# Kernel tuning notes

Measured on AMD Instinct MI355X. Metric: run time of the kernel, lower is better.

The kernel has to match this reference:

```python
import jax, jax.numpy as jnp
import numpy as np

D_IN = 2048
NUM_HEADS = 32
NUM_KV = 8
HEAD_DIM = 64
V_HEAD_DIM = 64
SEQ = 2048
BATCH = 1
EPS = 1e-6
NEG = -1e30


def setup_inputs() -> dict:
    key = jax.random.key(0)
    ks = jax.random.split(key, 10)
    x = jax.random.normal(ks[0], (BATCH, SEQ, D_IN), dtype=jnp.float32)
    # causal mask: True = masked out (upper triangle above diagonal)
    mask = jnp.triu(jnp.ones((SEQ, SEQ), dtype=jnp.bool_), k=1)
    # RoPE tables
    inv_freq = 1.0 / (10000.0 ** (jnp.arange(0, HEAD_DIM, 2, dtype=jnp.float32) / HEAD_DIM))
    t = jnp.arange(SEQ, dtype=jnp.float32)
    freqs = jnp.outer(t, inv_freq)  # (S, hd/2)
    emb = jnp.concatenate([freqs, freqs], axis=-1)  # (S, hd)
    cos = jnp.cos(emb)
    sin = jnp.sin(emb)
    scale = 0.02
    wq = jax.random.normal(ks[1], (D_IN, NUM_HEADS * HEAD_DIM), dtype=jnp.float32) * scale
    wk = jax.random.normal(ks[2], (D_IN, NUM_KV * HEAD_DIM), dtype=jnp.float32) * scale
    wv = jax.random.normal(ks[3], (D_IN, NUM_KV * V_HEAD_DIM), dtype=jnp.float32) * scale
    wo = jax.random.normal(ks[4], (NUM_HEADS * V_HEAD_DIM, D_IN), dtype=jnp.float32) * scale
    q_norm_w = jnp.ones((HEAD_DIM,), dtype=jnp.float32)
    k_norm_w = jnp.ones((HEAD_DIM,), dtype=jnp.float32)
    sink = jax.random.normal(ks[5], (NUM_HEADS,), dtype=jnp.float32) * 0.02
    return {"x": x, "mask": mask, "cos": cos, "sin": sin, "wq": wq, "wk": wk,
            "wv": wv, "wo": wo, "q_norm_w": q_norm_w, "k_norm_w": k_norm_w, "sink": sink}


def _rmsnorm(x, w):
    var = jnp.mean(jnp.square(x), axis=-1, keepdims=True)
    return x * jax.lax.rsqrt(var + EPS) * w


def _rope(x, cos, sin):
    # x: (b, h, s, d); cos/sin: (s, d)
    d = x.shape[-1]
    x1, x2 = x[..., : d // 2], x[..., d // 2:]
    rot = jnp.concatenate([-x2, x1], axis=-1)
    return x * cos[None, None] + rot * sin[None, None]


def reference(x, mask, cos, sin, wq, wk, wv, wo, q_norm_w, k_norm_w, sink):
    b, s, _ = x.shape
    rep = NUM_HEADS // NUM_KV
    q = (x @ wq).reshape(b, s, NUM_HEADS, HEAD_DIM).transpose(0, 2, 1, 3)
    k = (x @ wk).reshape(b, s, NUM_KV, HEAD_DIM).transpose(0, 2, 1, 3)
    v = (x @ wv).reshape(b, s, NUM_KV, V_HEAD_DIM).transpose(0, 2, 1, 3)
    q = _rope(_rmsnorm(q, q_norm_w), cos, sin)
    k = _rope(_rmsnorm(k, k_norm_w), cos, sin)
    k = jnp.repeat(k, rep, axis=1)  # (b, H, s, hd)
    v = jnp.repeat(v, rep, axis=1)  # (b, H, s, vd)
    scores = jnp.einsum('bhqd,bhkd->bhqk', q, k) * (HEAD_DIM ** -0.5)
    scores = jnp.where(mask[:s, :s], NEG, scores)
    # append learnable sink logit per head
    sink_col = jnp.broadcast_to(sink.reshape(1, NUM_HEADS, 1, 1), (b, NUM_HEADS, s, 1))
    scores = jnp.concatenate([scores, sink_col], axis=-1)
    weights = jax.nn.softmax(scores, axis=-1)[..., :-1]  # drop sink column
    out = jnp.einsum('bhqk,bhkd->bhqd', weights, v)
    out = out.transpose(0, 2, 1, 3).reshape(b, s, NUM_HEADS * V_HEAD_DIM)
    return out @ wo
```

## Files before the change

### kernel.cpp

```cpp
#include <hip/hip_runtime.h>

typedef unsigned short u16;
typedef __bf16 bf16;
typedef float f32x4 __attribute__((ext_vector_type(4)));
typedef bf16 bf16x8 __attribute__((ext_vector_type(8)));
typedef short s16x4 __attribute__((ext_vector_type(4)));
typedef u16 u16x4 __attribute__((ext_vector_type(4)));
typedef u16 u16x8 __attribute__((ext_vector_type(8)));

#define SEQ 2048
#define LOG2E 1.4426950408889634f

__device__ __forceinline__ u16 f2bf(float f) {
    return __builtin_bit_cast(u16, (bf16)f);
}
__device__ __forceinline__ float bf2f(u16 u) {
    unsigned int w = ((unsigned int)u) << 16;
    return __builtin_bit_cast(float, w);
}

__global__ __launch_bounds__(256) void cast_bf16_k(const float* __restrict__ in,
                                                   u16* __restrict__ out, int n4) {
    int i = blockIdx.x * 256 + threadIdx.x;
    int stride = gridDim.x * 256;
    for (; i < n4; i += stride) {
        float4 v = reinterpret_cast<const float4*>(in)[i];
        u16x4 o;
        o[0] = f2bf(v.x); o[1] = f2bf(v.y); o[2] = f2bf(v.z); o[3] = f2bf(v.w);
        reinterpret_cast<u16x4*>(out)[i] = o;
    }
}

__global__ __launch_bounds__(256) void transpose_cast_k(const float* __restrict__ src,
                                                        u16* __restrict__ dst, int R, int C) {
    __shared__ float t[64][65];
    int c0 = blockIdx.x * 64, r0 = blockIdx.y * 64;
    int tx = threadIdx.x & 63, ty = threadIdx.x >> 6;
#pragma unroll
    for (int i = 0; i < 16; ++i) {
        int r = ty + i * 4;
        t[r][tx] = src[(size_t)(r0 + r) * C + c0 + tx];
    }
    __syncthreads();
#pragma unroll
    for (int i = 0; i < 16; ++i) {
        int c = ty + i * 4;
        dst[(size_t)(c0 + c) * R + r0 + tx] = f2bf(t[tx][c]);
    }
}

__global__ __launch_bounds__(256) void gemm_bt_dbuf_k(const u16* __restrict__ A,
                                                      const u16* __restrict__ Bt,
                                                      u16* __restrict__ Cp,
                                                      int M, int N, int K) {
    __shared__ __align__(16) u16 As[2][128 * 32];
    __shared__ __align__(16) u16 Bs[2][128 * 32];
    int tid = threadIdx.x;
    int wave = tid >> 6, lane = tid & 63;
    int bm = blockIdx.y * 128, bn = blockIdx.x * 128;
    int z = blockIdx.z;
    int kt0 = z * (K >> 1), ktend = kt0 + (K >> 1);
    int wm = (wave >> 1) * 64, wn = (wave & 1) * 64;
    int g = lane >> 4, cidx = lane & 15;
    f32x4 acc[4][4] = {};

    int srow = lane >> 2;
    int skol = ((lane & 3) ^ ((srow >> 1) & 3)) * 8;
    int sl8 = (g ^ ((cidx >> 1) & 3)) * 8;

#define STAGE(buf, kt)                                                                \
    {                                                                                 \
        _Pragma("unroll")                                                             \
        for (int j = 0; j < 2; ++j) {                                                 \
            const u16* gpa = A + (size_t)(bm + (wave * 2 + j) * 16 + srow) * K + (kt) + skol; \
            __builtin_amdgcn_global_load_lds(                                         \
                (__attribute__((address_space(1))) void*)gpa,                         \
                (__attribute__((address_space(3))) void*)&As[buf][(wave * 2 + j) * 512], \
                16, 0, 0);                                                            \
        }                                                                             \
        _Pragma("unroll")                                                             \
        for (int j = 0; j < 2; ++j) {                                                 \
            const u16* gpb = Bt + (size_t)(bn + (wave * 2 + j) * 16 + srow) * K + (kt) + skol; \
            __builtin_amdgcn_global_load_lds(                                         \
                (__attribute__((address_space(1))) void*)gpb,                         \
                (__attribute__((address_space(3))) void*)&Bs[buf][(wave * 2 + j) * 512], \
                16, 0, 0);                                                            \
        }                                                                             \
    }

    STAGE(0, kt0);
    asm volatile("s_waitcnt vmcnt(0)" ::: "memory");
    __syncthreads();

    int cur = 0;
#pragma unroll 1
    for (int kt = kt0; kt < ktend; kt += 32) {
        if (kt + 32 < ktend) STAGE(cur ^ 1, kt + 32);

        bf16x8 af[4], bfr[4];
#pragma unroll
        for (int mi = 0; mi < 4; ++mi)
            af[mi] = *reinterpret_cast<const bf16x8*>(&As[cur][(wm + mi * 16 + cidx) * 32 + sl8]);
#pragma unroll
        for (int ni = 0; ni < 4; ++ni)
            bfr[ni] = *reinterpret_cast<const bf16x8*>(&Bs[cur][(wn + ni * 16 + cidx) * 32 + sl8]);
#pragma unroll
        for (int mi = 0; mi < 4; ++mi)
#pragma unroll
            for (int ni = 0; ni < 4; ++ni)
                acc[mi][ni] = __builtin_amdgcn_mfma_f32_16x16x32_bf16(af[mi], bfr[ni], acc[mi][ni], 0, 0, 0);

        asm volatile("s_waitcnt vmcnt(0)" ::: "memory");
        __syncthreads();
        cur ^= 1;
    }
#undef STAGE

    u16* cbase = Cp + (size_t)z * M * N;
#pragma unroll
    for (int mi = 0; mi < 4; ++mi) {
#pragma unroll
        for (int r = 0; r < 4; ++r) {
            int row = bm + wm + mi * 16 + g * 4 + r;
            u16* cp = cbase + (size_t)row * N + bn + wn + cidx;
#pragma unroll
            for (int ni = 0; ni < 4; ++ni)
                cp[ni * 16] = f2bf(acc[mi][ni][r]);
        }
    }
}

__global__ __launch_bounds__(256) void sum2_f32_k(const u16* __restrict__ a,
                                                  const u16* __restrict__ b,
                                                  float* __restrict__ out, int n8) {
    int i = blockIdx.x * 256 + threadIdx.x;
    if (i >= n8) return;
    u16x8 va = reinterpret_cast<const u16x8*>(a)[i];
    u16x8 vb = reinterpret_cast<const u16x8*>(b)[i];
    f32x4 lo, hi;
#pragma unroll
    for (int j = 0; j < 4; ++j) {
        lo[j] = bf2f(va[j]) + bf2f(vb[j]);
        hi[j] = bf2f(va[4 + j]) + bf2f(vb[4 + j]);
    }
    reinterpret_cast<f32x4*>(out)[i * 2] = lo;
    reinterpret_cast<f32x4*>(out)[i * 2 + 1] = hi;
}

__global__ __launch_bounds__(256) void norm_rope_k(const u16* __restrict__ p0,
                                                   const u16* __restrict__ p1,
                                                   const float* __restrict__ cosb,
                                                   const float* __restrict__ sinb,
                                                   const float* __restrict__ qw,
                                                   const float* __restrict__ kw,
                                                   u16* __restrict__ qn,
                                                   u16* __restrict__ kfrag) {
    int idx = blockIdx.x * 4 + (threadIdx.x >> 6);
    int lane = threadIdx.x & 63;
    int s = idx / 40, hh = idx - s * 40;
    size_t off = (hh < 32) ? ((size_t)s * 3072 + hh * 64 + lane)
                           : ((size_t)s * 3072 + 2048 + (hh - 32) * 64 + lane);
    float val = bf2f(p0[off]) + bf2f(p1[off]);
    float ss = val * val;
#pragma unroll
    for (int mm = 32; mm; mm >>= 1) ss += __shfl_xor(ss, mm);
    float w = (hh < 32) ? qw[lane] : kw[lane];
    float xn = val * rsqrtf(ss * (1.f / 64.f) + 1e-6f) * w;
    float part = __shfl_xor(xn, 32);
    float rot = (lane < 32) ? -part : part;
    float o = xn * cosb[s * 64 + lane] + rot * sinb[s * 64 + lane];
    if (hh < 32) {
        qn[(size_t)s * 2048 + hh * 64 + lane] = f2bf(o * (0.125f * LOG2E));
    } else {
        int h8 = hh - 32;
        kfrag[(((size_t)h8 * 128 + (s >> 4)) << 10) + (lane >> 3) * 128 + (s & 15) * 8 + (lane & 7)] = f2bf(o);
    }
}

__global__ __launch_bounds__(256) void v_frag_k(const u16* __restrict__ p0,
                                                const u16* __restrict__ p1,
                                                u16* __restrict__ vfrag) {
    __shared__ float t[64][65];
    int s0 = blockIdx.x * 64;
    int h = blockIdx.y;
    int tx = threadIdx.x & 63, ty = threadIdx.x >> 6;
#pragma unroll
    for (int i = 0; i < 16; ++i) {
        int r = ty + i * 4;
        size_t off = (size_t)(s0 + r) * 3072 + 2560 + h * 64 + tx;
        t[r][tx] = bf2f(p0[off]) + bf2f(p1[off]);
    }
    __syncthreads();
    int dt = threadIdx.x >> 6, g = (threadIdx.x >> 4) & 3, cc = threadIdx.x & 15;
#pragma unroll
    for (int kb2 = 0; kb2 < 4; ++kb2) {
        u16x4 o;
#pragma unroll
        for (int i = 0; i < 4; ++i) o[i] = f2bf(t[kb2 * 16 + g * 4 + i][dt * 16 + cc]);
        size_t idx = ((size_t)h * 64 + (s0 >> 5) + (kb2 >> 1)) * 2048 + dt * 512 + g * 128 + cc * 8 + (kb2 & 1) * 4;
        *reinterpret_cast<u16x4*>(&vfrag[idx]) = o;
    }
}

__global__ __launch_bounds__(256, 4) void attn_k(const u16* __restrict__ qn,
                                                 const u16* __restrict__ kfrag,
                                                 const u16* __restrict__ vfrag,
                                                 u16* __restrict__ obuf,
                                                 float* __restrict__ lbuf) {
    int h = blockIdx.x;
    int wave = threadIdx.x >> 6, lane = threadIdx.x & 63;
    int j = blockIdx.y * 4 + wave;
    int c, w;
    if (j < 32)       { c = j;                    w = 0; }
    else if (j < 96)  { c = 32 + ((j - 32) >> 1); w = (j - 32) & 1; }
    else if (j < 192) { int r = j - 96;  int q = r / 3; c = 64 + q; w = r - 3 * q; }
    else              { c = 96 + ((j - 192) >> 2); w = (j - 192) & 3; }

    int q0 = c * 16;
    int nk = q0 + 16;
    int kv0 = w * 512;
    int kvend = (kv0 + 512 < nk) ? (kv0 + 512) : nk;

    int kvh = h >> 2, g = lane >> 4, cc = lane & 15;
    int qrow = q0 + cc;

    const size_t qoff = (size_t)qrow * 2048 + h * 64;
    bf16x8 q_0 = *reinterpret_cast<const bf16x8*>(&qn[qoff + g * 8]);
    bf16x8 q_1 = *reinterpret_cast<const bf16x8*>(&qn[qoff + 32 + g * 8]);

    float l = 0.f;
    f32x4 o[4] = {};

    const u16* kbase = kfrag + (((size_t)kvh * 128) << 10) + lane * 8;
    const u16* vbase = vfrag + (size_t)kvh * 64 * 2048 + g * 128 + cc * 8;

    bf16x8 kf0[4], kf1[4];
#pragma unroll
    for (int sub = 0; sub < 4; ++sub) {
        const u16* kp = kbase + (size_t)((kv0 >> 4) + sub) * 1024;
        kf0[sub] = *reinterpret_cast<const bf16x8*>(kp);
        kf1[sub] = *reinterpret_cast<const bf16x8*>(kp + 512);
    }

#pragma unroll 1
    for (; kv0 < kvend; kv0 += 64) {
        f32x4 st[4];
        __builtin_amdgcn_s_setprio(1);
#pragma unroll
        for (int sub = 0; sub < 4; ++sub) {
            st[sub] = __builtin_amdgcn_mfma_f32_16x16x32_bf16(kf0[sub], q_0, (f32x4){0.f, 0.f, 0.f, 0.f}, 0, 0, 0);
            st[sub] = __builtin_amdgcn_mfma_f32_16x16x32_bf16(kf1[sub], q_1, st[sub], 0, 0, 0);
        }
        __builtin_amdgcn_s_setprio(0);

        if (kv0 + 64 < kvend) {
#pragma unroll
            for (int sub = 0; sub < 4; ++sub) {
                const u16* kp = kbase + (size_t)(((kv0 + 64) >> 4) + sub) * 1024;
                kf0[sub] = *reinterpret_cast<const bf16x8*>(kp);
                kf1[sub] = *reinterpret_cast<const bf16x8*>(kp + 512);
            }
        }

        bf16x8 vv[2][4];
#pragma unroll
        for (int sp = 0; sp < 2; ++sp)
#pragma unroll
            for (int dt = 0; dt < 4; ++dt)
                vv[sp][dt] = *reinterpret_cast<const bf16x8*>(
                    vbase + (size_t)((kv0 >> 5) + sp) * 2048 + dt * 512);

        if (kv0 + 64 > q0) {
#pragma unroll
            for (int sub = 0; sub < 4; ++sub)
#pragma unroll
                for (int r = 0; r < 4; ++r)
                    if (kv0 + sub * 16 + g * 4 + r > qrow) st[sub][r] = -1e30f;
        }

        s16x4 pf[4];
        float rs = 0.f;
#pragma unroll
        for (int sub = 0; sub < 4; ++sub)
#pragma unroll
            for (int r = 0; r < 4; ++r) {
                float e = __builtin_amdgcn_exp2f(st[sub][r]);
                rs += e;
                pf[sub][r] = (short)f2bf(e);
            }
        l += rs;

        __builtin_amdgcn_s_setprio(1);
#pragma unroll
        for (int sp = 0; sp < 2; ++sp)
#pragma unroll
            for (int dt = 0; dt < 4; ++dt) {
                s16x4 vlo = __builtin_bit_cast(s16x4,
                    __builtin_shufflevector(vv[sp][dt], vv[sp][dt], 0, 1, 2, 3));
                s16x4 vhi = __builtin_bit_cast(s16x4,
                    __builtin_shufflevector(vv[sp][dt], vv[sp][dt], 4, 5, 6, 7));
                o[dt] = __builtin_amdgcn_mfma_f32_16x16x16bf16_1k(vlo, pf[sp * 2], o[dt], 0, 0, 0);
                o[dt] = __builtin_amdgcn_mfma_f32_16x16x16bf16_1k(vhi, pf[sp * 2 + 1], o[dt], 0, 0, 0);
            }
        __builtin_amdgcn_s_setprio(0);
    }

    l += __shfl_xor(l, 16);
    l += __shfl_xor(l, 32);
    size_t slot = (size_t)h * 320 + j;
    if (lane < 16) lbuf[slot * 16 + cc] = l;
    u16* sp = obuf + slot * 1024;
#pragma unroll
    for (int dt = 0; dt < 4; ++dt) {
        u16x4 ov;
#pragma unroll
        for (int r = 0; r < 4; ++r) ov[r] = f2bf(o[dt][r]);
        *reinterpret_cast<u16x4*>(&sp[cc * 64 + dt * 16 + g * 4]) = ov;
    }
}

__global__ __launch_bounds__(256) void merge_k(const u16* __restrict__ obuf,
                                               const float* __restrict__ lbuf,
                                               const float* __restrict__ sink,
                                               u16* __restrict__ attnb) {
    int row = blockIdx.x;
    int c = row >> 4, cc = row & 15;
    int nw = (c >> 5) + 1;
    int jb = (c < 32) ? c
           : (c < 64) ? 32 + ((c - 32) << 1)
           : (c < 96) ? 96 + 3 * (c - 64)
                      : 192 + ((c - 96) << 2);
    int t = threadIdx.x;
    int h = t >> 3, col0 = (t & 7) * 8;

    float acc[8] = {};
    float lsum = __builtin_amdgcn_exp2f(sink[h] * LOG2E);
#pragma unroll 1
    for (int w = 0; w < nw; ++w) {
        size_t slot = (size_t)h * 320 + jb + w;
        lsum += lbuf[slot * 16 + cc];
        u16x8 v = *reinterpret_cast<const u16x8*>(&obuf[slot * 1024 + cc * 64 + col0]);
#pragma unroll
        for (int i = 0; i < 8; ++i) acc[i] += bf2f(v[i]);
    }
    float inv = 1.f / lsum;
    u16x8 ob;
#pragma unroll
    for (int i = 0; i < 8; ++i) ob[i] = f2bf(acc[i] * inv);
    *reinterpret_cast<u16x8*>(&attnb[(size_t)row * 2048 + h * 64 + col0]) = ob;
}

extern "C" void kernel_launch(void* const* d_in, const int* in_sizes, int n_in,
                              void* d_out, int out_size, void* d_ws, size_t ws_size,
                              hipStream_t stream) {
    const float* x    = (const float*)d_in[0];
    const float* cosb = (const float*)d_in[2];
    const float* sinb = (const float*)d_in[3];
    const float* wq   = (const float*)d_in[4];
    const float* wk   = (const float*)d_in[5];
    const float* wv   = (const float*)d_in[6];
    const float* wo   = (const float*)d_in[7];
    const float* qw   = (const float*)d_in[8];
    const float* kw   = (const float*)d_in[9];
    const float* sink = (const float*)d_in[10];
    float* out = (float*)d_out;

    char* ws = (char*)d_ws;
    size_t off = 0;
    auto alloc = [&](size_t bytes) {
        char* p = ws + off;
        off += (bytes + 255) & ~(size_t)255;
        return p;
    };
    u16*   xb    = (u16*)alloc((size_t)2048 * 2048 * 2);
    u16*   wqkvt = (u16*)alloc((size_t)3072 * 2048 * 2);
    u16*   wot   = (u16*)alloc((size_t)2048 * 2048 * 2);
    u16*   p0    = (u16*)alloc((size_t)2048 * 3072 * 2);
    u16*   p1    = (u16*)alloc((size_t)2048 * 3072 * 2);
    u16*   qnb   = (u16*)alloc((size_t)2048 * 2048 * 2);
    u16*   kfrag = (u16*)alloc((size_t)8 * 128 * 1024 * 2);
    u16*   vfrag = (u16*)alloc((size_t)8 * 64 * 2048 * 2);
    float* lbuf  = (float*)alloc((size_t)32 * 320 * 16 * 4);
    u16*   attnb = xb;
    u16*   obuf  = p0;
    u16*   o2p   = p0;

    cast_bf16_k<<<2048, 256, 0, stream>>>(x, xb, 2048 * 2048 / 4);
    transpose_cast_k<<<dim3(32, 32), 256, 0, stream>>>(wq, wqkvt, 2048, 2048);
    transpose_cast_k<<<dim3(8, 32), 256, 0, stream>>>(wk, wqkvt + (size_t)2048 * 2048, 2048, 512);
    transpose_cast_k<<<dim3(8, 32), 256, 0, stream>>>(wv, wqkvt + (size_t)2560 * 2048, 2048, 512);
    transpose_cast_k<<<dim3(32, 32), 256, 0, stream>>>(wo, wot, 2048, 2048);

    gemm_bt_dbuf_k<<<dim3(24, 16, 2), 256, 0, stream>>>(xb, wqkvt, p0, 2048, 3072, 2048);
    norm_rope_k<<<20480, 256, 0, stream>>>(p0, p1, cosb, sinb, qw, kw, qnb, kfrag);
    v_frag_k<<<dim3(32, 8), 256, 0, stream>>>(p0, p1, vfrag);

    attn_k<<<dim3(32, 80), 256, 0, stream>>>(qnb, kfrag, vfrag, obuf, lbuf);
    merge_k<<<2048, 256, 0, stream>>>(obuf, lbuf, sink, attnb);

    gemm_bt_dbuf_k<<<dim3(16, 16, 2), 256, 0, stream>>>(attnb, wot, o2p, 2048, 2048, 2048);
    sum2_f32_k<<<2048, 256, 0, stream>>>(o2p, o2p + (size_t)2048 * 2048, out, 2048 * 2048 / 8);
}
```

Measured before the change: 162.6 us.

## Use 16x16x32 MFMA for PV by permuting K/V fragment layouts; reverse block order

```diff
diff --git a/kernel.cpp b/kernel.cpp
--- a/kernel.cpp
+++ b/kernel.cpp
@@ -173,7 +173,10 @@
         qn[(size_t)s * 2048 + hh * 64 + lane] = f2bf(o * (0.125f * LOG2E));
     } else {
         int h8 = hh - 32;
-        kfrag[(((size_t)h8 * 128 + (s >> 4)) << 10) + (lane >> 3) * 128 + (s & 15) * 8 + (lane & 7)] = f2bf(o);
+        int k32 = s & 31;
+        int p32 = ((k32 >> 2) & 1) * 16 + ((k32 >> 3) << 2) + (k32 & 3);
+        int p = (s & ~31) + p32;
+        kfrag[(((size_t)h8 * 128 + (p >> 4)) << 10) + (lane >> 3) * 128 + (p & 15) * 8 + (lane & 7)] = f2bf(o);
     }
 }
 
@@ -193,12 +196,12 @@
     __syncthreads();
     int dt = threadIdx.x >> 6, g = (threadIdx.x >> 4) & 3, cc = threadIdx.x & 15;
 #pragma unroll
-    for (int kb2 = 0; kb2 < 4; ++kb2) {
-        u16x4 o;
-#pragma unroll
-        for (int i = 0; i < 4; ++i) o[i] = f2bf(t[kb2 * 16 + g * 4 + i][dt * 16 + cc]);
-        size_t idx = ((size_t)h * 64 + (s0 >> 5) + (kb2 >> 1)) * 2048 + dt * 512 + g * 128 + cc * 8 + (kb2 & 1) * 4;
-        *reinterpret_cast<u16x4*>(&vfrag[idx]) = o;
+    for (int kb = 0; kb < 2; ++kb) {
+        u16x8 o;
+#pragma unroll
+        for (int i = 0; i < 8; ++i) o[i] = f2bf(t[kb * 32 + g * 8 + i][dt * 16 + cc]);
+        *reinterpret_cast<u16x8*>(
+            &vfrag[((size_t)h * 64 + (s0 >> 5) + kb) * 2048 + dt * 512 + (size_t)(threadIdx.x & 63) * 8]) = o;
     }
 }
 
@@ -209,7 +212,7 @@
                                                  float* __restrict__ lbuf) {
     int h = blockIdx.x;
     int wave = threadIdx.x >> 6, lane = threadIdx.x & 63;
-    int j = blockIdx.y * 4 + wave;
+    int j = 319 - (blockIdx.y * 4 + wave);
     int c, w;
     if (j < 32)       { c = j;                    w = 0; }
     else if (j < 96)  { c = 32 + ((j - 32) >> 1); w = (j - 32) & 1; }
@@ -232,7 +235,7 @@
     f32x4 o[4] = {};
 
     const u16* kbase = kfrag + (((size_t)kvh * 128) << 10) + lane * 8;
-    const u16* vbase = vfrag + (size_t)kvh * 64 * 2048 + g * 128 + cc * 8;
+    const u16* vbase = vfrag + (size_t)kvh * 64 * 2048 + lane * 8;
 
     bf16x8 kf0[4], kf1[4];
 #pragma unroll
@@ -274,11 +277,13 @@
 #pragma unroll
             for (int sub = 0; sub < 4; ++sub)
 #pragma unroll
-                for (int r = 0; r < 4; ++r)
-                    if (kv0 + sub * 16 + g * 4 + r > qrow) st[sub][r] = -1e30f;
+                for (int r = 0; r < 4; ++r) {
+                    int key = kv0 + (sub >> 1) * 32 + g * 8 + (sub & 1) * 4 + r;
+                    if (key > qrow) st[sub][r] = -1e30f;
+                }
         }
 
-        s16x4 pf[4];
+        u16x8 pb[2];
         float rs = 0.f;
 #pragma unroll
         for (int sub = 0; sub < 4; ++sub)
@@ -286,22 +291,18 @@
             for (int r = 0; r < 4; ++r) {
                 float e = __builtin_amdgcn_exp2f(st[sub][r]);
                 rs += e;
-                pf[sub][r] = (short)f2bf(e);
+                pb[sub >> 1][(sub & 1) * 4 + r] = f2bf(e);
             }
         l += rs;
 
         __builtin_amdgcn_s_setprio(1);
 #pragma unroll
-        for (int sp = 0; sp < 2; ++sp)
-#pragma unroll
-            for (int dt = 0; dt < 4; ++dt) {
-                s16x4 vlo = __builtin_bit_cast(s16x4,
-                    __builtin_shufflevector(vv[sp][dt], vv[sp][dt], 0, 1, 2, 3));
-                s16x4 vhi = __builtin_bit_cast(s16x4,
-                    __builtin_shufflevector(vv[sp][dt], vv[sp][dt], 4, 5, 6, 7));
-                o[dt] = __builtin_amdgcn_mfma_f32_16x16x16bf16_1k(vlo, pf[sp * 2], o[dt], 0, 0, 0);
-                o[dt] = __builtin_amdgcn_mfma_f32_16x16x16bf16_1k(vhi, pf[sp * 2 + 1], o[dt], 0, 0, 0);
-            }
+        for (int sp = 0; sp < 2; ++sp) {
+            bf16x8 pbb = __builtin_bit_cast(bf16x8, pb[sp]);
+#pragma unroll
+            for (int dt = 0; dt < 4; ++dt)
+                o[dt] = __builtin_amdgcn_mfma_f32_16x16x32_bf16(vv[sp][dt], pbb, o[dt], 0, 0, 0);
+        }
         __builtin_amdgcn_s_setprio(0);
     }
 
```

Result: no change. 163.5 us (+0.5%).
